# Performance work log

Measured on AMD Instinct MI355X. Metric: run time of the kernel, lower is better.

## Reference

```python
import jax, jax.numpy as jnp
import numpy as np

# ---- static module config (matches init_kwargs) ----
N = 16384
E_DIM = 256
SHARE_N_E = 2048
SPECIFIC = [1024, 1024, 1024]
TOTAL_N_E = SHARE_N_E + sum(SPECIFIC)  # 5120
BETA = 0.25
NUM_MOD = len(SPECIFIC)
BIG = 1e7  # value written into masked-out distance entries

# prefix boundaries of the per-modality code blocks: [2048, 3072, 4096, 5120]
CODE_BOUNDS = jnp.asarray(np.cumsum([SHARE_N_E] + SPECIFIC)[:, None].squeeze(-1) if False else np.cumsum([SHARE_N_E] + SPECIFIC), dtype=jnp.int32)
# code -> modality id; shared codes get -1
CODE_MOD = jnp.searchsorted(CODE_BOUNDS, jnp.arange(TOTAL_N_E, dtype=jnp.int32), side='right') - 1  # [TOTAL_N_E]


def setup_inputs() -> dict:
    key = jax.random.key(0)
    k1, k2 = jax.random.split(key)
    x = jax.random.normal(k1, (N, E_DIM), dtype=jnp.float32)
    emb_weight = jax.random.normal(k2, (TOTAL_N_E, E_DIM), dtype=jnp.float32)  # nn.Embedding default N(0,1)
    split_index = jnp.array([0, 5120, 10240, 16384], dtype=jnp.int64)  # 3 equal modality segments
    return {"x": x, "emb_weight": emb_weight, "split_index": split_index}


def reference(x, emb_weight, split_index):
    # pairwise squared distances d[n, c] = ||x_n||^2 + ||e_c||^2 - 2 x_n . e_c
    d = (jnp.sum(x * x, axis=1, keepdims=True)
         + jnp.sum(emb_weight * emb_weight, axis=1)[None, :]
         - 2.0 * jnp.einsum('nd,cd->nc', x, emb_weight))  # [N, TOTAL_N_E]

    # token -> modality id via split boundaries (vectorized form of the Python loop)
    tok_mod = jnp.searchsorted(split_index, jnp.arange(N, dtype=split_index.dtype), side='right') - 1  # [N]
    tok_mod = tok_mod.astype(jnp.int32)
    # allowed = shared code OR code's modality matches token's modality
    allowed = (CODE_MOD[None, :] == -1) | (CODE_MOD[None, :] == tok_mod[:, None])  # [N, TOTAL_N_E]
    d = jnp.where(allowed, d, jnp.float32(BIG))

    indices = jnp.argmin(d, axis=-1)              # [N]
    x_q = jnp.take(emb_weight, indices, axis=0)   # [N, E_DIM]

    # per-modality VQ losses: codebook + beta * commitment (mse over segment)
    sg = jax.lax.stop_gradient
    se_commit = jnp.sum((sg(x_q) - x) ** 2, axis=1)   # [N]
    se_code = jnp.sum((x_q - sg(x)) ** 2, axis=1)     # [N]
    seg_commit = jax.ops.segment_sum(se_commit, tok_mod, num_segments=NUM_MOD)
    seg_code = jax.ops.segment_sum(se_code, tok_mod, num_segments=NUM_MOD)
    counts = (split_index[1:] - split_index[:-1]).astype(jnp.float32) * jnp.float32(E_DIM)
    q_losses = seg_code / counts + BETA * (seg_commit / counts)  # [NUM_MOD]

    # straight-through estimator
    x_q_ste = x + sg(x_q - x)
    return (x_q_ste, indices, d, q_losses)
```

## Files before the change

kernel.cpp:

```cpp
#include <hip/hip_runtime.h>
#include <stdint.h>

#define N_TOK    16384
#define E_DIM    256
#define N_CODE   5120
#define N_SHARED 2048
#define BIGF     1e7f

#define BM  128
#define BN  128
#define BK  32
#define NCB (N_CODE / BN)
#define NKT (E_DIM / BK)
#define CHUNK (BM * BK)
#define NBLK (NCB * (N_TOK / BM))

#define IDX_OFF ((size_t)N_TOK * E_DIM)
#define D_OFF   (IDX_OFF + N_TOK)
#define QL_OFF  (D_OFF + (size_t)N_TOK * N_CODE)

typedef float f32x4 __attribute__((ext_vector_type(4)));
typedef short bf16x8 __attribute__((ext_vector_type(8)));
typedef short s16x4 __attribute__((ext_vector_type(4)));

typedef __attribute__((address_space(1))) const unsigned int g_u32;
typedef __attribute__((address_space(3))) unsigned int lds_u32;

#define VMW(n) asm volatile("s_waitcnt vmcnt(" #n ")" ::: "memory")

__device__ __forceinline__ unsigned short bf16_rn(float f) {
    unsigned u = __float_as_uint(f);
    u += 0x7FFF + ((u >> 16) & 1);
    return (unsigned short)(u >> 16);
}
__device__ __forceinline__ float bf16_to_f(unsigned short h) {
    return __uint_as_float(((unsigned)h) << 16);
}

__global__ __launch_bounds__(256) void convert_kernel(const float* __restrict__ x,
                                                      const float* __restrict__ emb,
                                                      float* __restrict__ xx,
                                                      float* __restrict__ ee,
                                                      short* __restrict__ xhi, short* __restrict__ xlo,
                                                      short* __restrict__ ehi, short* __restrict__ elo) {
    int wid = threadIdx.x >> 6, ln = threadIdx.x & 63;
    int row = blockIdx.x * 4 + wid;
    const float* src; float* nrm; short *hiA, *loA; int rl, tb;
    if (row < N_TOK) {
        src = x + (size_t)row * E_DIM; nrm = xx + row;
        tb = row >> 7; rl = row & 127; hiA = xhi; loA = xlo;
    } else {
        int r = row - N_TOK;
        src = emb + (size_t)r * E_DIM; nrm = ee + r;
        tb = r >> 7; rl = r & 127; hiA = ehi; loA = elo;
    }
    f32x4 v = ((const f32x4*)src)[ln];
    float s = v[0]*v[0] + v[1]*v[1] + v[2]*v[2] + v[3]*v[3];
    s16x4 h, l;
#pragma unroll
    for (int c = 0; c < 4; ++c) {
        unsigned short hh = bf16_rn(v[c]);
        h[c] = (short)hh;
        l[c] = (short)bf16_rn(v[c] - bf16_to_f(hh));
    }
    int kt = ln >> 3, q = (ln >> 1) & 3, kl4 = (ln & 1) * 4;
    size_t di = ((((size_t)tb * NKT + kt) * 4 + q) * BM + rl) * 8 + kl4;
    *(s16x4*)&hiA[di] = h;
    *(s16x4*)&loA[di] = l;
#pragma unroll
    for (int sh = 32; sh; sh >>= 1) s += __shfl_xor(s, sh, 64);
    if (ln == 0) *nrm = s;
}

__global__ __launch_bounds__(256, 2) void gemm_kernel(const short* __restrict__ xhi,
                                                      const short* __restrict__ xlo,
                                                      const short* __restrict__ ehi,
                                                      const short* __restrict__ elo,
                                                      const int* __restrict__ split,
                                                      const float* __restrict__ xx,
                                                      const float* __restrict__ ee,
                                                      float* __restrict__ out,
                                                      float* __restrict__ pmin,
                                                      int*   __restrict__ pidx) {
    __shared__ short Ah[2][CHUNK], Bh[2][CHUNK];
    __shared__ short Al[2][CHUNK], Bl[2][CHUNK];
    __shared__ float xxs[BM];
    __shared__ float ees[BN];
    __shared__ float redv[2][BM];
    __shared__ int   redi[2][BM];

    const int lin = blockIdx.y * NCB + blockIdx.x;
    const int s_  = (lin & 7) * (NBLK / 8) + (lin >> 3);
    const int bx = s_ % NCB;
    const int by = s_ / NCB;
    const int m0 = by * BM, n0 = bx * BN;
    const int t = threadIdx.x;

    const int s1 = split[1], s2v = split[2];
    const int tmFirst = (m0 >= s1) + (m0 >= s2v);
    const int cmod = (n0 < N_SHARED) ? -1 : ((n0 - N_SHARED) >> 10);

    float* dOut = out + D_OFF;

    if (cmod >= 0 && cmod != tmFirst) {
        f32x4 big = {BIGF, BIGF, BIGF, BIGF};
#pragma unroll
        for (int u = 0; u < 16; ++u) {
            int idx = u * 256 + t;
            int row = idx >> 5, col4 = idx & 31;
            __builtin_nontemporal_store(big,
                (f32x4*)(dOut + (size_t)(m0 + row) * N_CODE + n0) + col4);
        }
        if (t < BM) {
            pmin[(size_t)(m0 + t) * NCB + bx] = BIGF;
            pidx[(size_t)(m0 + t) * NCB + bx] = n0;
        }
        return;
    }

    if (t < BM) xxs[t] = xx[m0 + t];
    else        ees[t - BM] = ee[n0 + (t - BM)];
    __syncthreads();

    f32x4 acc[4][4] = {};

    const int wid = t >> 6, lane = t & 63;
    const int quad = lane >> 4, ln16 = lane & 15;
    const int wr = (wid >> 1) * 64, wc = (wid & 1) * 64;
    const int qb = quad * BM;

    const short* aHiG = xhi + (size_t)by * NKT * CHUNK;
    const short* aLoG = xlo + (size_t)by * NKT * CHUNK;
    const short* bHiG = ehi + (size_t)bx * NKT * CHUNK;
    const short* bLoG = elo + (size_t)bx * NKT * CHUNK;
    const int tOff = t * 8;

    auto stageU0 = [&](int kt, int b) {
        const size_t co = (size_t)kt * CHUNK;
#pragma unroll
        for (int p = 0; p < 2; ++p) {
            int o = p * 2048 + tOff;
            __builtin_amdgcn_global_load_lds((g_u32*)(aHiG + co + o), (lds_u32*)&Ah[b][o], 16, 0, 0);
            __builtin_amdgcn_global_load_lds((g_u32*)(bHiG + co + o), (lds_u32*)&Bh[b][o], 16, 0, 0);
        }
    };
    auto stageU1 = [&](int kt, int b) {
        const size_t co = (size_t)kt * CHUNK;
#pragma unroll
        for (int p = 0; p < 2; ++p) {
            int o = p * 2048 + tOff;
            __builtin_amdgcn_global_load_lds((g_u32*)(aLoG + co + o), (lds_u32*)&Al[b][o], 16, 0, 0);
            __builtin_amdgcn_global_load_lds((g_u32*)(bLoG + co + o), (lds_u32*)&Bl[b][o], 16, 0, 0);
        }
    };

    stageU0(0, 0); stageU1(0, 0); stageU0(1, 1);
    int cur = 0;

#define TILE(VA, VB, DOU1, DOU2, KT)                                                         \
    {                                                                                        \
        VMW(VA);                                                                             \
        __builtin_amdgcn_s_barrier();                                                        \
        if (DOU1) stageU1((KT) + 1, cur ^ 1);                                                \
        bf16x8 ah[4], bh[4];                                                                 \
        _Pragma("unroll") for (int i = 0; i < 4; ++i)                                        \
            ah[i] = *(const bf16x8*)&Ah[cur][(qb + wr + i * 16 + ln16) * 8];                 \
        _Pragma("unroll") for (int j = 0; j < 4; ++j)                                        \
            bh[j] = *(const bf16x8*)&Bh[cur][(qb + wc + j * 16 + ln16) * 8];                 \
        __builtin_amdgcn_s_setprio(1);                                                       \
        _Pragma("unroll") for (int i = 0; i < 4; ++i)                                        \
            _Pragma("unroll") for (int j = 0; j < 4; ++j)                                    \
                acc[i][j] = __builtin_amdgcn_mfma_f32_16x16x32_bf16(bh[j], ah[i], acc[i][j], 0, 0, 0); \
        __builtin_amdgcn_s_setprio(0);                                                       \
        VMW(VB);                                                                             \
        __builtin_amdgcn_s_barrier();                                                        \
        if (DOU2) stageU0((KT) + 2, cur);                                                    \
        bf16x8 bl[4];                                                                        \
        _Pragma("unroll") for (int j = 0; j < 4; ++j)                                        \
            bl[j] = *(const bf16x8*)&Bl[cur][(qb + wc + j * 16 + ln16) * 8];                 \
        __builtin_amdgcn_s_setprio(1);                                                       \
        _Pragma("unroll") for (int i = 0; i < 4; ++i)                                        \
            _Pragma("unroll") for (int j = 0; j < 4; ++j)                                    \
                acc[i][j] = __builtin_amdgcn_mfma_f32_16x16x32_bf16(bl[j], ah[i], acc[i][j], 0, 0, 0); \
        __builtin_amdgcn_s_setprio(0);                                                       \
        bf16x8 al[4];                                                                        \
        _Pragma("unroll") for (int i = 0; i < 4; ++i)                                        \
            al[i] = *(const bf16x8*)&Al[cur][(qb + wr + i * 16 + ln16) * 8];                 \
        __builtin_amdgcn_s_setprio(1);                                                       \
        _Pragma("unroll") for (int i = 0; i < 4; ++i)                                        \
            _Pragma("unroll") for (int j = 0; j < 4; ++j)                                    \
                acc[i][j] = __builtin_amdgcn_mfma_f32_16x16x32_bf16(bh[j], al[i], acc[i][j], 0, 0, 0); \
        __builtin_amdgcn_s_setprio(0);                                                       \
        cur ^= 1;                                                                            \
    }

    for (int kt = 0; kt < NKT - 2; ++kt)
        TILE(8, 8, true, true, kt);
    TILE(8, 8, true, false, NKT - 2);
    TILE(4, 0, false, false, NKT - 1);
#undef TILE

#pragma unroll
    for (int i = 0; i < 4; ++i) {
        const int lt = wr + i * 16 + ln16;
        const int gt = m0 + lt;
        const float xv = xxs[lt];
        float best = 3.4e38f;
        int bidx = n0;
#pragma unroll
        for (int j = 0; j < 4; ++j) {
            const int cb = wc + j * 16 + quad * 4;
            f32x4 dv;
#pragma unroll
            for (int r = 0; r < 4; ++r) {
                float v = fmaf(-2.f, acc[i][j][r], xv + ees[cb + r]);
                dv[r] = v;
                if (v < best) { best = v; bidx = n0 + cb + r; }
            }
            __builtin_nontemporal_store(dv, (f32x4*)(dOut + (size_t)gt * N_CODE + n0 + cb));
        }
#pragma unroll
        for (int s = 16; s < 64; s <<= 1) {
            float ov = __shfl_xor(best, s, 64);
            int   oi = __shfl_xor(bidx, s, 64);
            if (ov < best || (ov == best && oi < bidx)) { best = ov; bidx = oi; }
        }
        if (quad == 0) { redv[wid & 1][lt] = best; redi[wid & 1][lt] = bidx; }
    }
    __syncthreads();
    if (t < BM) {
        float v0 = redv[0][t]; int i0 = redi[0][t];
        float v1 = redv[1][t]; int i1 = redi[1][t];
        if (v1 < v0 || (v1 == v0 && i1 < i0)) { v0 = v1; i0 = i1; }
        pmin[(size_t)(m0 + t) * NCB + bx] = v0;
        pidx[(size_t)(m0 + t) * NCB + bx] = i0;
    }
}

__global__ __launch_bounds__(256) void gather_kernel(const float* __restrict__ x,
                                                     const float* __restrict__ emb,
                                                     const int* __restrict__ split,
                                                     float* __restrict__ out,
                                                     const float* __restrict__ pmin,
                                                     const int* __restrict__ pidx,
                                                     float* __restrict__ wsLoss) {
    __shared__ float ls[3];
    int t = threadIdx.x, wid = t >> 6, ln = t & 63;
    if (t < 3) ls[t] = 0.f;
    __syncthreads();
    int tok = blockIdx.x * 4 + wid;

    float best = 3.4e38f;
    int bi = 0x7fffffff;
    if (ln < NCB) {
        best = pmin[(size_t)tok * NCB + ln];
        bi   = pidx[(size_t)tok * NCB + ln];
    }
#pragma unroll
    for (int sh = 32; sh; sh >>= 1) {
        float ov = __shfl_xor(best, sh, 64);
        int   oi = __shfl_xor(bi, sh, 64);
        if (ov < best || (ov == best && oi < bi)) { best = ov; bi = oi; }
    }
    if (ln == 0) out[IDX_OFF + tok] = (float)bi;
    int idx = bi;

    f32x4 e  = ((const f32x4*)(emb + (size_t)idx * E_DIM))[ln];
    f32x4 xv = ((const f32x4*)(x + (size_t)tok * E_DIM))[ln];
    f32x4 q;
    float s = 0.f;
#pragma unroll
    for (int c = 0; c < 4; ++c) {
        float d = e[c] - xv[c];
        q[c] = xv[c] + d;
        s = fmaf(d, d, s);
    }
    __builtin_nontemporal_store(q, (f32x4*)(out + (size_t)tok * E_DIM) + ln);
#pragma unroll
    for (int sh = 32; sh; sh >>= 1) s += __shfl_xor(s, sh, 64);
    if (ln == 0) {
        int mod = (tok >= split[1]) + (tok >= split[2]);
        atomicAdd(&ls[mod], s);
    }
    __syncthreads();
    if (t < 3) wsLoss[blockIdx.x * 3 + t] = ls[t];
}

__global__ __launch_bounds__(256) void loss_kernel(const float* __restrict__ wsLoss,
                                                   const int* __restrict__ split,
                                                   float* __restrict__ out, int nblk) {
    __shared__ float red[256];
    float s[3] = {0.f, 0.f, 0.f};
    for (int b = threadIdx.x; b < nblk; b += 256) {
        s[0] += wsLoss[b * 3 + 0];
        s[1] += wsLoss[b * 3 + 1];
        s[2] += wsLoss[b * 3 + 2];
    }
    for (int m = 0; m < 3; ++m) {
        red[threadIdx.x] = s[m];
        __syncthreads();
        for (int st = 128; st; st >>= 1) {
            if (threadIdx.x < st) red[threadIdx.x] += red[threadIdx.x + st];
            __syncthreads();
        }
        if (threadIdx.x == 0) {
            float cnt = (float)(split[m + 1] - split[m]) * (float)E_DIM;
            float a = red[0] / cnt;
            out[QL_OFF + m] = a + 0.25f * a;
        }
        __syncthreads();
    }
}

extern "C" void kernel_launch(void* const* d_in, const int* in_sizes, int n_in,
                              void* d_out, int out_size, void* d_ws, size_t ws_size,
                              hipStream_t stream) {
    const float* x   = (const float*)d_in[0];
    const float* emb = (const float*)d_in[1];
    const int* split = (const int*)d_in[2];
    float* out = (float*)d_out;

    float* xx     = (float*)d_ws;
    float* ee     = xx + N_TOK;
    float* wsLoss = ee + N_CODE;
    float* pmin   = wsLoss + 4096 * 3;
    int*   pidx   = (int*)(pmin + (size_t)N_TOK * NCB);
    short* xhi    = (short*)(pidx + (size_t)N_TOK * NCB);
    short* xlo    = xhi + (size_t)N_TOK * E_DIM;
    short* ehi    = xlo + (size_t)N_TOK * E_DIM;
    short* elo    = ehi + (size_t)N_CODE * E_DIM;
    int nblkGather = N_TOK / 4;

    convert_kernel<<<dim3((N_TOK + N_CODE) / 4), dim3(256), 0, stream>>>(x, emb, xx, ee, xhi, xlo, ehi, elo);
    gemm_kernel<<<dim3(NCB, N_TOK / BM), dim3(256), 0, stream>>>(xhi, xlo, ehi, elo, split, xx, ee, out, pmin, pidx);
    gather_kernel<<<dim3(nblkGather), dim3(256), 0, stream>>>(x, emb, split, out, pmin, pidx, wsLoss);
    loss_kernel<<<dim3(1), dim3(256), 0, stream>>>(wsLoss, split, out, nblkGather);
}
```

Baseline: 427.9 us.

## Replace double-buffered LDS pipeline with single-buffer loop to raise occupancy

Removes the hand-scheduled double-buffered global-to-LDS pipeline and its manual vmcnt waits. Each k-step now loads all four hi/lo tiles into a single LDS buffer between two __syncthreads. Launch bounds go from 2 to 3 blocks per CU, relying on the halved LDS footprint and extra resident waves to hide load latency. The cost is that loads no longer overlap MFMA work within a block, and register pressure may rise under the tighter bound.

```diff
diff --git a/kernel.cpp b/kernel.cpp
--- a/kernel.cpp
+++ b/kernel.cpp
@@ -25,8 +25,6 @@
 
 typedef __attribute__((address_space(1))) const unsigned int g_u32;
 typedef __attribute__((address_space(3))) unsigned int lds_u32;
-
-#define VMW(n) asm volatile("s_waitcnt vmcnt(" #n ")" ::: "memory")
 
 __device__ __forceinline__ unsigned short bf16_rn(float f) {
     unsigned u = __float_as_uint(f);
@@ -72,7 +70,7 @@
     if (ln == 0) *nrm = s;
 }
 
-__global__ __launch_bounds__(256, 2) void gemm_kernel(const short* __restrict__ xhi,
+__global__ __launch_bounds__(256, 3) void gemm_kernel(const short* __restrict__ xhi,
                                                       const short* __restrict__ xlo,
                                                       const short* __restrict__ ehi,
                                                       const short* __restrict__ elo,
@@ -82,8 +80,8 @@
                                                       float* __restrict__ out,
                                                       float* __restrict__ pmin,
                                                       int*   __restrict__ pidx) {
-    __shared__ short Ah[2][CHUNK], Bh[2][CHUNK];
-    __shared__ short Al[2][CHUNK], Bl[2][CHUNK];
+    __shared__ short Ah[CHUNK], Bh[CHUNK];
+    __shared__ short Al[CHUNK], Bl[CHUNK];
     __shared__ float xxs[BM];
     __shared__ float ees[BN];
     __shared__ float redv[2][BM];
@@ -120,7 +118,6 @@
 
     if (t < BM) xxs[t] = xx[m0 + t];
     else        ees[t - BM] = ee[n0 + (t - BM)];
-    __syncthreads();
 
     f32x4 acc[4][4] = {};
 
@@ -135,70 +132,58 @@
     const short* bLoG = elo + (size_t)bx * NKT * CHUNK;
     const int tOff = t * 8;
 
-    auto stageU0 = [&](int kt, int b) {
+    for (int kt = 0; kt < NKT; ++kt) {
+        __syncthreads();
         const size_t co = (size_t)kt * CHUNK;
 #pragma unroll
         for (int p = 0; p < 2; ++p) {
             int o = p * 2048 + tOff;
-            __builtin_amdgcn_global_load_lds((g_u32*)(aHiG + co + o), (lds_u32*)&Ah[b][o], 16, 0, 0);
-            __builtin_amdgcn_global_load_lds((g_u32*)(bHiG + co + o), (lds_u32*)&Bh[b][o], 16, 0, 0);
-        }
-    };
-    auto stageU1 = [&](int kt, int b) {
-        const size_t co = (size_t)kt * CHUNK;
-#pragma unroll
-        for (int p = 0; p < 2; ++p) {
-            int o = p * 2048 + tOff;
-            __builtin_amdgcn_global_load_lds((g_u32*)(aLoG + co + o), (lds_u32*)&Al[b][o], 16, 0, 0);
-            __builtin_amdgcn_global_load_lds((g_u32*)(bLoG + co + o), (lds_u32*)&Bl[b][o], 16, 0, 0);
-        }
-    };
-
-    stageU0(0, 0); stageU1(0, 0); stageU0(1, 1);
-    int cur = 0;
-
-#define TILE(VA, VB, DOU1, DOU2, KT)                                                         \
-    {                                                                                        \
-        VMW(VA);                                                                             \
-        __builtin_amdgcn_s_barrier();                                                        \
-        if (DOU1) stageU1((KT) + 1, cur ^ 1);                                                \
-        bf16x8 ah[4], bh[4];                                                                 \
-        _Pragma("unroll") for (int i = 0; i < 4; ++i)                                        \
-            ah[i] = *(const bf16x8*)&Ah[cur][(qb + wr + i * 16 + ln16) * 8];                 \
-        _Pragma("unroll") for (int j = 0; j < 4; ++j)                                        \
-            bh[j] = *(const bf16x8*)&Bh[cur][(qb + wc + j * 16 + ln16) * 8];                 \
-        __builtin_amdgcn_s_setprio(1);                                                       \
-        _Pragma("unroll") for (int i = 0; i < 4; ++i)                                        \
-            _Pragma("unroll") for (int j = 0; j < 4; ++j)                                    \
-                acc[i][j] = __builtin_amdgcn_mfma_f32_16x16x32_bf16(bh[j], ah[i], acc[i][j], 0, 0, 0); \
-        __builtin_amdgcn_s_setprio(0);                                                       \
-        VMW(VB);                                                                             \
-        __builtin_amdgcn_s_barrier();                                                        \
-        if (DOU2) stageU0((KT) + 2, cur);                                                    \
-        bf16x8 bl[4];                                                                        \
-        _Pragma("unroll") for (int j = 0; j < 4; ++j)                                        \
-            bl[j] = *(const bf16x8*)&Bl[cur][(qb + wc + j * 16 + ln16) * 8];                 \
-        __builtin_amdgcn_s_setprio(1);                                                       \
-        _Pragma("unroll") for (int i = 0; i < 4; ++i)                                        \
-            _Pragma("unroll") for (int j = 0; j < 4; ++j)                                    \
-                acc[i][j] = __builtin_amdgcn_mfma_f32_16x16x32_bf16(bl[j], ah[i], acc[i][j], 0, 0, 0); \
-        __builtin_amdgcn_s_setprio(0);                                                       \
-        bf16x8 al[4];                                                                        \
-        _Pragma("unroll") for (int i = 0; i < 4; ++i)                                        \
-            al[i] = *(const bf16x8*)&Al[cur][(qb + wr + i * 16 + ln16) * 8];                 \
-        __builtin_amdgcn_s_setprio(1);                                                       \
-        _Pragma("unroll") for (int i = 0; i < 4; ++i)                                        \
-            _Pragma("unroll") for (int j = 0; j < 4; ++j)                                    \
-                acc[i][j] = __builtin_amdgcn_mfma_f32_16x16x32_bf16(bh[j], al[i], acc[i][j], 0, 0, 0); \
-        __builtin_amdgcn_s_setprio(0);                                                       \
-        cur ^= 1;                                                                            \
-    }
-
-    for (int kt = 0; kt < NKT - 2; ++kt)
-        TILE(8, 8, true, true, kt);
-    TILE(8, 8, true, false, NKT - 2);
-    TILE(4, 0, false, false, NKT - 1);
-#undef TILE
+            __builtin_amdgcn_global_load_lds((g_u32*)(aHiG + co + o), (lds_u32*)&Ah[o], 16, 0, 0);
+            __builtin_amdgcn_global_load_lds((g_u32*)(bHiG + co + o), (lds_u32*)&Bh[o], 16, 0, 0);
+            __builtin_amdgcn_global_load_lds((g_u32*)(aLoG + co + o), (lds_u32*)&Al[o], 16, 0, 0);
+            __builtin_amdgcn_global_load_lds((g_u32*)(bLoG + co + o), (lds_u32*)&Bl[o], 16, 0, 0);
+        }
+        __syncthreads();
+
+        bf16x8 ah[4], bh[4];
+#pragma unroll
+        for (int i = 0; i < 4; ++i)
+            ah[i] = *(const bf16x8*)&Ah[(qb + wr + i * 16 + ln16) * 8];
+#pragma unroll
+        for (int j = 0; j < 4; ++j)
+            bh[j] = *(const bf16x8*)&Bh[(qb + wc + j * 16 + ln16) * 8];
+        __builtin_amdgcn_s_setprio(1);
+#pragma unroll
+        for (int i = 0; i < 4; ++i)
+#pragma unroll
+            for (int j = 0; j < 4; ++j)
+                acc[i][j] = __builtin_amdgcn_mfma_f32_16x16x32_bf16(bh[j], ah[i], acc[i][j], 0, 0, 0);
+        __builtin_amdgcn_s_setprio(0);
+
+        bf16x8 bl[4];
+#pragma unroll
+        for (int j = 0; j < 4; ++j)
+            bl[j] = *(const bf16x8*)&Bl[(qb + wc + j * 16 + ln16) * 8];
+        __builtin_amdgcn_s_setprio(1);
+#pragma unroll
+        for (int i = 0; i < 4; ++i)
+#pragma unroll
+            for (int j = 0; j < 4; ++j)
+                acc[i][j] = __builtin_amdgcn_mfma_f32_16x16x32_bf16(bl[j], ah[i], acc[i][j], 0, 0, 0);
+        __builtin_amdgcn_s_setprio(0);
+
+        bf16x8 al[4];
+#pragma unroll
+        for (int i = 0; i < 4; ++i)
+            al[i] = *(const bf16x8*)&Al[(qb + wr + i * 16 + ln16) * 8];
+        __builtin_amdgcn_s_setprio(1);
+#pragma unroll
+        for (int i = 0; i < 4; ++i)
+#pragma unroll
+            for (int j = 0; j < 4; ++j)
+                acc[i][j] = __builtin_amdgcn_mfma_f32_16x16x32_bf16(bh[j], al[i], acc[i][j], 0, 0, 0);
+        __builtin_amdgcn_s_setprio(0);
+    }
 
 #pragma unroll
     for (int i = 0; i < 4; ++i) {
```

Result: no change. 421.7 us (-1.5%).
